# Performance work log

Measured on AMD Instinct MI355X. Metric: run time of the kernel, lower is better.

The kernel has to match this reference:

```python
import jax, jax.numpy as jnp
import numpy as np

EMBED_DIM = 1024
NUM_HEADS = 16
HEAD_DIM = EMBED_DIM // NUM_HEADS


def setup_inputs() -> dict:
    key = jax.random.key(0)
    ks = jax.random.split(key, 5)
    B, N = 4, 2048
    s_in = 1.0 / np.sqrt(EMBED_DIM)
    return {
        "x": jax.random.normal(ks[0], (B, N, EMBED_DIM), dtype=jnp.float32),
        "qkv_w": jax.random.uniform(ks[1], (3 * EMBED_DIM, EMBED_DIM), jnp.float32, -s_in, s_in),
        "qkv_b": jax.random.uniform(ks[2], (3 * EMBED_DIM,), jnp.float32, -s_in, s_in),
        "o_w": jax.random.uniform(ks[3], (EMBED_DIM, EMBED_DIM), jnp.float32, -s_in, s_in),
        "o_b": jax.random.uniform(ks[4], (EMBED_DIM,), jnp.float32, -s_in, s_in),
    }


def reference(x, qkv_w, qkv_b, o_w, o_b):
    B, N, E = x.shape
    H, D = NUM_HEADS, HEAD_DIM
    # qkv: [B, N, 3E] -> [B, N, H, 3D] -> [B, H, N, 3D], then chunk last dim
    qkv = (jnp.einsum('bne,fe->bnf', x, qkv_w) + qkv_b)
    qkv = qkv.reshape(B, N, H, 3 * D).transpose(0, 2, 1, 3)
    q, k, v = jnp.split(qkv, 3, axis=-1)
    scale = 1.0 / np.sqrt(D)
    scores = jnp.einsum('bhqd,bhkd->bhqk', q, k) * scale
    attn = jax.nn.softmax(scores, axis=-1)  # dropout is identity in eval mode
    out = jnp.einsum('bhqk,bhkd->bhqd', attn, v)
    out = out.transpose(0, 2, 1, 3).reshape(B, N, E)
    return jnp.einsum('bne,fe->bnf', out, o_w) + o_b
```

## Files before the change

kernel.cpp:

```cpp
#include <hip/hip_runtime.h>

typedef unsigned short u16;
typedef float f32x4 __attribute__((ext_vector_type(4)));
typedef float f32x16 __attribute__((ext_vector_type(16)));
typedef short bf16x8 __attribute__((ext_vector_type(8)));
typedef int i32x2 __attribute__((ext_vector_type(2)));

__device__ __forceinline__ u16 f2bf(float f){
  union { float f; unsigned u; } x; x.f = f;
  unsigned r = (x.u + 0x7FFFu + ((x.u >> 16) & 1u)) >> 16;
  return (u16)r;
}

__device__ __forceinline__ unsigned cvtpk(float lo, float hi){
  unsigned r;
  asm("v_cvt_pk_bf16_f32 %0, %1, %2" : "=v"(r) : "v"(lo), "v"(hi));
  return r;
}

__device__ __forceinline__ void exp4q(float& a, float& b, float& c, float& d){
  asm("v_exp_f32 %0, %0\n\t"
      "v_exp_f32 %1, %1\n\t"
      "v_exp_f32 %2, %2\n\t"
      "v_exp_f32 %3, %3\n\t"
      "s_nop 1"
      : "+v"(a), "+v"(b), "+v"(c), "+v"(d));
}

__device__ __forceinline__ f32x4 mfma_bf16(bf16x8 a, bf16x8 b, f32x4 c){
  return __builtin_amdgcn_mfma_f32_16x16x32_bf16(a, b, c, 0, 0, 0);
}

__device__ __forceinline__ f32x16 mfma32(bf16x8 a, bf16x8 b, f32x16 c){
  return __builtin_amdgcn_mfma_f32_32x32x16_bf16(a, b, c, 0, 0, 0);
}

__device__ __forceinline__ void gload16(const u16* g, u16* l){
  __builtin_amdgcn_global_load_lds((__attribute__((address_space(1))) void*)g,
                                   (__attribute__((address_space(3))) void*)l, 16, 0, 0);
}

__global__ void cvt_bf16(const float* __restrict__ in, u16* __restrict__ out, int n4){
  int stride = gridDim.x * blockDim.x;
  for (int i = blockIdx.x*blockDim.x + threadIdx.x; i < n4; i += stride){
    float4 v = ((const float4*)in)[i];
    ushort4 o;
    o.x = f2bf(v.x); o.y = f2bf(v.y); o.z = f2bf(v.z); o.w = f2bf(v.w);
    ((ushort4*)out)[i] = o;
  }
}

template<int NCH, int NTHR>
__device__ __forceinline__ void stage32(const u16* src, int ld, u16* lds, int tid){
#pragma unroll
  for (int i = 0; i < NCH/NTHR; i++){
    int c = i*NTHR + tid;
    int row = c >> 2, slot = c & 3;
    int col = ((slot ^ (row & 3)) << 3);
    gload16(src + (size_t)row*ld + col, lds + ((size_t)(c & ~63) << 3));
  }
}

template<int NTHR>
__device__ __forceinline__ void stage64(const u16* src, int ld, u16* lds, int tid){
#pragma unroll
  for (int i = 0; i < 512/NTHR; i++){
    int c = i*NTHR + tid;
    int row = c >> 3, slot = c & 7;
    int col = ((slot ^ (row & 7)) << 3);
    gload16(src + (size_t)row*ld + col, lds + ((size_t)(c & ~63) << 3));
  }
}

template<int MODE, int WROWS>
__launch_bounds__(WROWS*128)
__global__ void gemm_bt(const u16* __restrict__ A, const u16* __restrict__ Bw,
                        const float* __restrict__ bias,
                        u16* __restrict__ Qp, u16* __restrict__ Kp, u16* __restrict__ Vt,
                        float* __restrict__ Co, int M, int Nf, int K)
{
  constexpr int BM = WROWS*64;
  constexpr int NTHR = WROWS*128;
  __shared__ u16 lsA[2][BM*32];
  __shared__ u16 lsB[2][128*32];
  int tid = threadIdx.x;
  int wave = tid >> 6, lane = tid & 63, grp = lane >> 4, l16 = lane & 15;
  int ntn = Nf >> 7;
  int bm = blockIdx.x / ntn, bn = blockIdx.x % ntn;
  const u16* Ab = A + (size_t)bm*BM*K;
  const u16* Bb = Bw + (size_t)bn*128*K;
  int wm = wave >> 1, wn = wave & 1;
  f32x4 acc[4][4] = {};

  stage32<BM*4, NTHR>(Ab, K, lsA[0], tid);
  stage32<512,  NTHR>(Bb, K, lsB[0], tid);
  int nk = K >> 5;
  for (int t = 0; t < nk; t++){
    __syncthreads();
    int cur = t & 1;
    if (t + 1 < nk){
      stage32<BM*4, NTHR>(Ab + ((t+1) << 5), K, lsA[cur^1], tid);
      stage32<512,  NTHR>(Bb + ((t+1) << 5), K, lsB[cur^1], tid);
    }
    const u16* la = lsA[cur];
    const u16* lb = lsB[cur];
    bf16x8 af[4], bfr[4];
#pragma unroll
    for (int mf = 0; mf < 4; mf++){
      int row = wm*64 + mf*16 + l16;
      af[mf] = *(const bf16x8*)(la + row*32 + ((grp ^ (row & 3)) << 3));
    }
#pragma unroll
    for (int nf = 0; nf < 4; nf++){
      int row = wn*64 + nf*16 + l16;
      bfr[nf] = *(const bf16x8*)(lb + row*32 + ((grp ^ (row & 3)) << 3));
    }
#pragma unroll
    for (int mf = 0; mf < 4; mf++)
#pragma unroll
      for (int nf = 0; nf < 4; nf++)
        acc[mf][nf] = mfma_bf16(af[mf], bfr[nf], acc[mf][nf]);
  }

  int mrow0 = bm*BM + wm*64;
  int f0 = bn*128 + wn*64;
#pragma unroll
  for (int nf = 0; nf < 4; nf++){
    int f = f0 + nf*16 + l16;
    float bv = bias[f];
    if constexpr (MODE == 0){
      int h = f / 192, c = f % 192;
#pragma unroll
      for (int mf = 0; mf < 4; mf++){
        int mbase = mrow0 + mf*16 + grp*4;
        int bb = mbase >> 11, n0 = mbase & 2047;
        size_t bh = (size_t)bb*16 + h;
        if (c >= 128){
          ushort4 w;
          w.x = f2bf(acc[mf][nf][0] + bv);
          w.y = f2bf(acc[mf][nf][1] + bv);
          w.z = f2bf(acc[mf][nf][2] + bv);
          w.w = f2bf(acc[mf][nf][3] + bv);
          *(ushort4*)(Vt + (bh*64 + (size_t)(c - 128))*2048 + n0) = w;
        } else {
          u16* dst = (c < 64) ? Qp : Kp;
          float sc = (c < 64) ? 0.18033688011f : 1.0f;
          int cc = c & 63;
#pragma unroll
          for (int r = 0; r < 4; r++)
            dst[(bh*2048 + n0 + r)*64 + cc] = f2bf((acc[mf][nf][r] + bv) * sc);
        }
      }
    } else {
#pragma unroll
      for (int mf = 0; mf < 4; mf++){
        int mbase = mrow0 + mf*16 + grp*4;
#pragma unroll
        for (int r = 0; r < 4; r++)
          Co[(size_t)(mbase + r)*Nf + f] = acc[mf][nf][r] + bv;
      }
    }
  }
}

__device__ __forceinline__ bf16x8 packP(const f32x16& pp, int base){
  unsigned t0 = cvtpk(pp[base+0], pp[base+1]);
  unsigned t1 = cvtpk(pp[base+2], pp[base+3]);
  unsigned t2 = cvtpk(pp[base+4], pp[base+5]);
  unsigned t3 = cvtpk(pp[base+6], pp[base+7]);
  i32x2 r02 = __builtin_amdgcn_permlane32_swap((int)t0, (int)t2, false, false);
  i32x2 r13 = __builtin_amdgcn_permlane32_swap((int)t1, (int)t3, false, false);
  union { unsigned u[4]; bf16x8 v; } pu;
  pu.u[0] = (unsigned)r02.x;
  pu.u[1] = (unsigned)r13.x;
  pu.u[2] = (unsigned)r02.y;
  pu.u[3] = (unsigned)r13.y;
  return pu.v;
}

__device__ __forceinline__ void expv16(f32x16& p){
#pragma unroll
  for (int r = 0; r < 16; r += 4){
    float a = p[r], b = p[r+1], c = p[r+2], d = p[r+3];
    exp4q(a, b, c, d);
    p[r] = a; p[r+1] = b; p[r+2] = c; p[r+3] = d;
  }
}

__launch_bounds__(512, 4)
__global__ void attn_fwd(const u16* __restrict__ Qg, const u16* __restrict__ Kg,
                         const u16* __restrict__ Vtg, u16* __restrict__ Oa)
{
  __shared__ u16 kl[4][64*64];
  __shared__ u16 vl[4][64*64];
  int tid = threadIdx.x;
  int lane = tid & 63, wave = tid >> 6;
  int q32 = lane & 31, hi = lane >> 5;
  int bid = (blockIdx.x & 7) * 64 + (blockIdx.x >> 3);
  int bh = bid >> 3, qt = bid & 7;
  int b = bh >> 4, h = bh & 15;
  int q0 = qt*256 + wave*32;
  const u16* Qb = Qg + ((size_t)bh*2048 + q0)*64;
  const u16* Kb = Kg + (size_t)bh*2048*64;
  const u16* Vb = Vtg + (size_t)bh*64*2048;

  bf16x8 qf[4];
#pragma unroll
  for (int s = 0; s < 4; s++)
    qf[s] = *(const bf16x8*)(Qb + q32*64 + s*16 + hi*8);

  f32x16 lacc = {};
  f32x16 oacc[2] = {};

#pragma unroll
  for (int t = 0; t < 3; t++){
    stage64<512>(Kb + (size_t)t*64*64, 64, kl[t], tid);
    stage64<512>(Vb + t*64, 2048, vl[t], tid);
  }

  for (int kt = 0; kt < 32; kt++){
    if (kt < 30)       asm volatile("s_waitcnt vmcnt(4)" ::: "memory");
    else if (kt == 30) asm volatile("s_waitcnt vmcnt(2)" ::: "memory");
    else               asm volatile("s_waitcnt vmcnt(0)" ::: "memory");
    __builtin_amdgcn_s_barrier();
    __builtin_amdgcn_sched_barrier(0);
    if (kt + 3 < 32){
      stage64<512>(Kb + (size_t)(kt+3)*64*64, 64, kl[(kt+3)&3], tid);
      stage64<512>(Vb + (kt+3)*64, 2048, vl[(kt+3)&3], tid);
    }
    const u16* lk = kl[kt & 3];
    const u16* lv = vl[kt & 3];

    f32x16 p0 = {}, p1 = {};
    __builtin_amdgcn_s_setprio(1);
#pragma unroll
    for (int s = 0; s < 4; s++){
      int r0 = q32;
      bf16x8 k0 = *(const bf16x8*)(lk + r0*64 + (((s*2+hi) ^ (r0 & 7)) << 3));
      p0 = mfma32(k0, qf[s], p0);
      int r1 = 32 + q32;
      bf16x8 k1 = *(const bf16x8*)(lk + r1*64 + (((s*2+hi) ^ (r1 & 7)) << 3));
      p1 = mfma32(k1, qf[s], p1);
    }
    __builtin_amdgcn_s_setprio(0);

    expv16(p0); expv16(p1);
#pragma unroll
    for (int r = 0; r < 16; r++) lacc[r] += p0[r];
#pragma unroll
    for (int r = 0; r < 16; r++) lacc[r] += p1[r];

#pragma unroll
    for (int ks = 0; ks < 4; ks++){
      bf16x8 pb = packP((ks < 2) ? p0 : p1, (ks & 1) * 8);
      __builtin_amdgcn_s_setprio(1);
      int rowd0 = q32;
      bf16x8 v0 = *(const bf16x8*)(lv + rowd0*64 + (((ks*2+hi) ^ (rowd0 & 7)) << 3));
      oacc[0] = mfma32(v0, pb, oacc[0]);
      int rowd1 = 32 + q32;
      bf16x8 v1 = *(const bf16x8*)(lv + rowd1*64 + (((ks*2+hi) ^ (rowd1 & 7)) << 3));
      oacc[1] = mfma32(v1, pb, oacc[1]);
      __builtin_amdgcn_s_setprio(0);
    }
  }

#pragma unroll
  for (int r = 0; r < 8; r++) lacc[r] += lacc[r+8];
#pragma unroll
  for (int r = 0; r < 4; r++) lacc[r] += lacc[r+4];
  float l = (lacc[0] + lacc[1]) + (lacc[2] + lacc[3]);
  l += __shfl_xor(l, 32, 64);
  float inv = 1.0f / l;

  size_t obase = ((size_t)b*2048 + q0 + q32)*1024 + h*64;
#pragma unroll
  for (int dblk = 0; dblk < 2; dblk++)
#pragma unroll
    for (int rb = 0; rb < 4; rb++){
      ushort4 w;
      w.x = f2bf(oacc[dblk][rb*4+0] * inv);
      w.y = f2bf(oacc[dblk][rb*4+1] * inv);
      w.z = f2bf(oacc[dblk][rb*4+2] * inv);
      w.w = f2bf(oacc[dblk][rb*4+3] * inv);
      *(ushort4*)(Oa + obase + dblk*32 + rb*8 + hi*4) = w;
    }
}

extern "C" void kernel_launch(void* const* d_in, const int* in_sizes, int n_in,
                              void* d_out, int out_size, void* d_ws, size_t ws_size,
                              hipStream_t stream)
{
  const float* x    = (const float*)d_in[0];
  const float* qkvw = (const float*)d_in[1];
  const float* qkvb = (const float*)d_in[2];
  const float* ow   = (const float*)d_in[3];
  const float* ob   = (const float*)d_in[4];
  float* out = (float*)d_out;

  u16* xb = (u16*)d_ws;
  u16* wq = xb + (size_t)8192*1024;
  u16* wo = wq + (size_t)3072*1024;
  u16* Qp = wo + (size_t)1024*1024;
  u16* Kp = Qp + (size_t)64*2048*64;
  u16* Vt = Kp + (size_t)64*2048*64;
  u16* Oa = Vt + (size_t)64*2048*64;

  cvt_bf16<<<1024, 256, 0, stream>>>(x, xb, (8192*1024)/4);
  cvt_bf16<<<512, 256, 0, stream>>>(qkvw, wq, (3072*1024)/4);
  cvt_bf16<<<256, 256, 0, stream>>>(ow, wo, (1024*1024)/4);

  gemm_bt<0,2><<<64*24, 256, 0, stream>>>(xb, wq, qkvb, Qp, Kp, Vt, nullptr, 8192, 3072, 1024);
  attn_fwd<<<512, 512, 0, stream>>>(Qp, Kp, Vt, Oa);
  gemm_bt<1,2><<<64*8, 256, 0, stream>>>(Oa, wo, ob, nullptr, nullptr, nullptr, out, 8192, 1024, 1024);
}
```

Measured before the change: 196.2 us.

## Replace QKV GEMM with 256x256-tile, 8-wave, quarter-staged pipelined kernel

Adds a dedicated QKV projection kernel that uses 256x256 output tiles with BK=64, 512 threads, and double-buffered LDS. Global loads are staged in quarters, interleaved with the MFMA phases and gated by explicit vmcnt waits. It also remaps block IDs into XCD-friendly groups and raises wave priority around the MFMA bursts. The goals are more data reuse per tile, fewer blocks, and overlap of loads with compute. The cost is heavy register pressure (single occupancy) and a small grid of 384 blocks on 256 CUs, which leaves a wave-quantization tail.

```diff
diff --git a/kernel.cpp b/kernel.cpp
--- a/kernel.cpp
+++ b/kernel.cpp
@@ -72,35 +72,31 @@
   }
 }
 
-template<int MODE, int WROWS>
-__launch_bounds__(WROWS*128)
-__global__ void gemm_bt(const u16* __restrict__ A, const u16* __restrict__ Bw,
-                        const float* __restrict__ bias,
-                        u16* __restrict__ Qp, u16* __restrict__ Kp, u16* __restrict__ Vt,
-                        float* __restrict__ Co, int M, int Nf, int K)
+__launch_bounds__(256)
+__global__ void gemm_bt1(const u16* __restrict__ A, const u16* __restrict__ Bw,
+                         const float* __restrict__ bias, float* __restrict__ Co,
+                         int M, int Nf, int K)
 {
-  constexpr int BM = WROWS*64;
-  constexpr int NTHR = WROWS*128;
-  __shared__ u16 lsA[2][BM*32];
+  __shared__ u16 lsA[2][128*32];
   __shared__ u16 lsB[2][128*32];
   int tid = threadIdx.x;
   int wave = tid >> 6, lane = tid & 63, grp = lane >> 4, l16 = lane & 15;
   int ntn = Nf >> 7;
   int bm = blockIdx.x / ntn, bn = blockIdx.x % ntn;
-  const u16* Ab = A + (size_t)bm*BM*K;
+  const u16* Ab = A + (size_t)bm*128*K;
   const u16* Bb = Bw + (size_t)bn*128*K;
   int wm = wave >> 1, wn = wave & 1;
   f32x4 acc[4][4] = {};
 
-  stage32<BM*4, NTHR>(Ab, K, lsA[0], tid);
-  stage32<512,  NTHR>(Bb, K, lsB[0], tid);
+  stage32<512,256>(Ab, K, lsA[0], tid);
+  stage32<512,256>(Bb, K, lsB[0], tid);
   int nk = K >> 5;
   for (int t = 0; t < nk; t++){
     __syncthreads();
     int cur = t & 1;
     if (t + 1 < nk){
-      stage32<BM*4, NTHR>(Ab + ((t+1) << 5), K, lsA[cur^1], tid);
-      stage32<512,  NTHR>(Bb + ((t+1) << 5), K, lsB[cur^1], tid);
+      stage32<512,256>(Ab + ((t+1) << 5), K, lsA[cur^1], tid);
+      stage32<512,256>(Bb + ((t+1) << 5), K, lsB[cur^1], tid);
     }
     const u16* la = lsA[cur];
     const u16* lb = lsB[cur];
@@ -122,42 +118,181 @@
         acc[mf][nf] = mfma_bf16(af[mf], bfr[nf], acc[mf][nf]);
   }
 
-  int mrow0 = bm*BM + wm*64;
+  int mrow0 = bm*128 + wm*64;
   int f0 = bn*128 + wn*64;
 #pragma unroll
   for (int nf = 0; nf < 4; nf++){
     int f = f0 + nf*16 + l16;
     float bv = bias[f];
-    if constexpr (MODE == 0){
-      int h = f / 192, c = f % 192;
-#pragma unroll
-      for (int mf = 0; mf < 4; mf++){
-        int mbase = mrow0 + mf*16 + grp*4;
-        int bb = mbase >> 11, n0 = mbase & 2047;
-        size_t bh = (size_t)bb*16 + h;
-        if (c >= 128){
-          ushort4 w;
-          w.x = f2bf(acc[mf][nf][0] + bv);
-          w.y = f2bf(acc[mf][nf][1] + bv);
-          w.z = f2bf(acc[mf][nf][2] + bv);
-          w.w = f2bf(acc[mf][nf][3] + bv);
-          *(ushort4*)(Vt + (bh*64 + (size_t)(c - 128))*2048 + n0) = w;
-        } else {
-          u16* dst = (c < 64) ? Qp : Kp;
-          float sc = (c < 64) ? 0.18033688011f : 1.0f;
-          int cc = c & 63;
-#pragma unroll
-          for (int r = 0; r < 4; r++)
-            dst[(bh*2048 + n0 + r)*64 + cc] = f2bf((acc[mf][nf][r] + bv) * sc);
-        }
-      }
-    } else {
-#pragma unroll
-      for (int mf = 0; mf < 4; mf++){
-        int mbase = mrow0 + mf*16 + grp*4;
+#pragma unroll
+    for (int mf = 0; mf < 4; mf++){
+      int mbase = mrow0 + mf*16 + grp*4;
+#pragma unroll
+      for (int r = 0; r < 4; r++)
+        Co[(size_t)(mbase + r)*Nf + f] = acc[mf][nf][r] + bv;
+    }
+  }
+}
+
+__launch_bounds__(512, 1)
+__global__ void gemm_qkv(const u16* __restrict__ A, const u16* __restrict__ Bw,
+                         const float* __restrict__ bias,
+                         u16* __restrict__ Qp, u16* __restrict__ Kp,
+                         u16* __restrict__ Vt, int M, int Nf, int K)
+{
+  __shared__ u16 lsA[2][256*64];
+  __shared__ u16 lsB[2][256*64];
+  int tid = threadIdx.x;
+  int lane = tid & 63, grp = lane >> 4, l16 = lane & 15;
+  int wave = tid >> 6;
+  int wr = wave >> 2, wc = wave & 3;
+  int ntn = Nf >> 8;
+  int bid = (blockIdx.x & 7) * 48 + (blockIdx.x >> 3);
+  int bm = bid / ntn, bn = bid % ntn;
+  const u16* Ab = A + (size_t)bm*256*K;
+  const u16* Bb = Bw + (size_t)bn*256*K;
+
+  f32x4 acc[8][4] = {};
+
+  auto stageHalf = [&](const u16* src, u16* lds, int h){
+#pragma unroll
+    for (int i = 0; i < 2; i++){
+      int c = i*512 + tid;
+      int row = h*128 + (c >> 3);
+      int col = (((c & 7) ^ (row & 7)) << 3);
+      gload16(src + (size_t)row*K + col, lds + h*8192 + ((size_t)(c & ~63) << 3));
+    }
+  };
+
+  stageHalf(Ab, lsA[0], 0);
+  stageHalf(Bb, lsB[0], 0);
+  stageHalf(Ab, lsA[0], 1);
+  stageHalf(Bb, lsB[0], 1);
+  asm volatile("s_waitcnt vmcnt(4)" ::: "memory");
+
+  int nkt = K >> 6;
+  for (int t = 0; t < nkt; t++){
+    const u16* la = lsA[t & 1];
+    const u16* lb = lsB[t & 1];
+    const u16* As = Ab + ((t+1) << 6);
+    const u16* Bs = Bb + ((t+1) << 6);
+    u16* dA = lsA[(t+1) & 1];
+    u16* dB = lsB[(t+1) & 1];
+    bool pf = (t + 1) < nkt;
+    bf16x8 af[4][2], bf[2][2];
+
+    __builtin_amdgcn_s_barrier();
+#pragma unroll
+    for (int m = 0; m < 4; m++){
+      int grow = (m*2 + wr)*16 + l16;
+#pragma unroll
+      for (int ks = 0; ks < 2; ks++)
+        af[m][ks] = *(const bf16x8*)(la + grow*64 + (((ks*4+grp) ^ (grow & 7)) << 3));
+    }
+#pragma unroll
+    for (int n = 0; n < 2; n++){
+      int brow = (n*4 + wc)*16 + l16;
+#pragma unroll
+      for (int ks = 0; ks < 2; ks++)
+        bf[n][ks] = *(const bf16x8*)(lb + brow*64 + (((ks*4+grp) ^ (brow & 7)) << 3));
+    }
+    if (pf) stageHalf(As, dA, 0);
+    __builtin_amdgcn_s_setprio(1);
+#pragma unroll
+    for (int m = 0; m < 4; m++)
+#pragma unroll
+      for (int n = 0; n < 2; n++)
+#pragma unroll
+        for (int ks = 0; ks < 2; ks++)
+          acc[m][n] = mfma_bf16(af[m][ks], bf[n][ks], acc[m][n]);
+    __builtin_amdgcn_s_setprio(0);
+    if (pf) asm volatile("s_waitcnt vmcnt(4)" ::: "memory");
+    else    asm volatile("s_waitcnt vmcnt(2)" ::: "memory");
+
+    __builtin_amdgcn_s_barrier();
+#pragma unroll
+    for (int m = 0; m < 4; m++){
+      int grow = ((m+4)*2 + wr)*16 + l16;
+#pragma unroll
+      for (int ks = 0; ks < 2; ks++)
+        af[m][ks] = *(const bf16x8*)(la + grow*64 + (((ks*4+grp) ^ (grow & 7)) << 3));
+    }
+    if (pf) stageHalf(Bs, dB, 0);
+    __builtin_amdgcn_s_setprio(1);
+#pragma unroll
+    for (int m = 0; m < 4; m++)
+#pragma unroll
+      for (int n = 0; n < 2; n++)
+#pragma unroll
+        for (int ks = 0; ks < 2; ks++)
+          acc[m+4][n] = mfma_bf16(af[m][ks], bf[n][ks], acc[m+4][n]);
+    __builtin_amdgcn_s_setprio(0);
+    if (pf) asm volatile("s_waitcnt vmcnt(4)" ::: "memory");
+    else    asm volatile("s_waitcnt vmcnt(0)" ::: "memory");
+
+    __builtin_amdgcn_s_barrier();
+#pragma unroll
+    for (int n = 0; n < 2; n++){
+      int brow = ((n+2)*4 + wc)*16 + l16;
+#pragma unroll
+      for (int ks = 0; ks < 2; ks++)
+        bf[n][ks] = *(const bf16x8*)(lb + brow*64 + (((ks*4+grp) ^ (brow & 7)) << 3));
+    }
+    if (pf) stageHalf(As, dA, 1);
+    __builtin_amdgcn_s_setprio(1);
+#pragma unroll
+    for (int m = 0; m < 4; m++)
+#pragma unroll
+      for (int n = 0; n < 2; n++)
+#pragma unroll
+        for (int ks = 0; ks < 2; ks++)
+          acc[m+4][n+2] = mfma_bf16(af[m][ks], bf[n][ks], acc[m+4][n+2]);
+    __builtin_amdgcn_s_setprio(0);
+
+#pragma unroll
+    for (int m = 0; m < 4; m++){
+      int grow = (m*2 + wr)*16 + l16;
+#pragma unroll
+      for (int ks = 0; ks < 2; ks++)
+        af[m][ks] = *(const bf16x8*)(la + grow*64 + (((ks*4+grp) ^ (grow & 7)) << 3));
+    }
+    if (pf) stageHalf(Bs, dB, 1);
+    __builtin_amdgcn_s_setprio(1);
+#pragma unroll
+    for (int m = 0; m < 4; m++)
+#pragma unroll
+      for (int n = 0; n < 2; n++)
+#pragma unroll
+        for (int ks = 0; ks < 2; ks++)
+          acc[m][n+2] = mfma_bf16(af[m][ks], bf[n][ks], acc[m][n+2]);
+    __builtin_amdgcn_s_setprio(0);
+    if (pf) asm volatile("s_waitcnt vmcnt(4)" ::: "memory");
+  }
+
+#pragma unroll
+  for (int n = 0; n < 4; n++){
+    int f = bn*256 + (n*4 + wc)*16 + l16;
+    float bv = bias[f];
+    int h = f / 192, c = f % 192;
+#pragma unroll
+    for (int m = 0; m < 8; m++){
+      int mbase = bm*256 + (m*2 + wr)*16 + grp*4;
+      int bb = mbase >> 11, n0 = mbase & 2047;
+      size_t bh = (size_t)bb*16 + h;
+      if (c >= 128){
+        ushort4 w;
+        w.x = f2bf(acc[m][n][0] + bv);
+        w.y = f2bf(acc[m][n][1] + bv);
+        w.z = f2bf(acc[m][n][2] + bv);
+        w.w = f2bf(acc[m][n][3] + bv);
+        *(ushort4*)(Vt + (bh*64 + (size_t)(c - 128))*2048 + n0) = w;
+      } else {
+        u16* dst = (c < 64) ? Qp : Kp;
+        float sc = (c < 64) ? 0.18033688011f : 1.0f;
+        int cc = c & 63;
 #pragma unroll
         for (int r = 0; r < 4; r++)
-          Co[(size_t)(mbase + r)*Nf + f] = acc[mf][nf][r] + bv;
+          dst[(bh*2048 + n0 + r)*64 + cc] = f2bf((acc[m][n][r] + bv) * sc);
       }
     }
   }
@@ -309,7 +444,7 @@
   cvt_bf16<<<512, 256, 0, stream>>>(qkvw, wq, (3072*1024)/4);
   cvt_bf16<<<256, 256, 0, stream>>>(ow, wo, (1024*1024)/4);
 
-  gemm_bt<0,2><<<64*24, 256, 0, stream>>>(xb, wq, qkvb, Qp, Kp, Vt, nullptr, 8192, 3072, 1024);
+  gemm_qkv<<<32*12, 512, 0, stream>>>(xb, wq, qkvb, Qp, Kp, Vt, 8192, 3072, 1024);
   attn_fwd<<<512, 512, 0, stream>>>(Qp, Kp, Vt, Oa);
-  gemm_bt<1,2><<<64*8, 256, 0, stream>>>(Oa, wo, ob, nullptr, nullptr, nullptr, out, 8192, 1024, 1024);
-}
+  gemm_bt1<<<64*8, 256, 0, stream>>>(Oa, wo, ob, out, 8192, 1024, 1024);
+}
```

Measured after the change: 193.6 us. About the same (-1.3%).
